# Kernel optimization log

Measured on AMD Instinct MI355X. Metric: run time of the kernel, lower is better.

## Reference

```python
import jax, jax.numpy as jnp
import numpy as np

H = 1024          # hidden_dim
N_AVAIL = 32768   # number of available ops (rows of the score matrix)
N_M = 64          # machines
N_OP = 40000      # unfinished ops
N_JOB = 2000      # jobs
L = 4             # policy_num_layers


def setup_inputs() -> dict:
    key = jax.random.key(0)
    ks = jax.random.split(key, 12)
    s_in = (2.0 / (2 * H + 2)) ** 0.5   # kaiming-ish scale
    s_h = (2.0 / H) ** 0.5
    return {
        "x_m": jax.random.normal(ks[0], (N_M, H), jnp.float32),
        "x_op": jax.random.normal(ks[1], (N_OP, H), jnp.float32),
        "job_srpt": jax.random.uniform(ks[2], (N_JOB,), jnp.float32),
        "pt": jax.random.uniform(ks[3], (N_AVAIL,), jnp.float32),  # process_time / max_process_time
        "W0": jax.random.normal(ks[4], (2 * H + 2, H), jnp.float32) * s_in,
        "b0": jnp.zeros((H,), jnp.float32),
        "W1": jax.random.normal(ks[5], (H, H), jnp.float32) * s_h,
        "b1": jnp.zeros((H,), jnp.float32),
        "W2": jax.random.normal(ks[6], (H, H), jnp.float32) * s_h,
        "b2": jnp.zeros((H,), jnp.float32),
        "W3": jax.random.normal(ks[7], (H, 1), jnp.float32) * s_h,
        "b3": jnp.zeros((1,), jnp.float32),
        "m_ids": jax.random.randint(ks[8], (N_AVAIL,), 0, N_M, jnp.int32),
        "op_idx": jax.random.randint(ks[9], (N_AVAIL,), 0, N_OP, jnp.int32),
        "job_ids": jax.random.randint(ks[10], (N_AVAIL,), 0, N_JOB, jnp.int32),
    }


def reference(x_m, x_op, job_srpt, pt, W0, b0, W1, b1, W2, b2, W3, b3,
              m_ids, op_idx, job_ids):
    # Batched gather + concat: replaces the per-op Python loop of torch.cat's.
    feat = jnp.concatenate(
        [x_m[m_ids],                     # [N, H]
         x_op[op_idx],                   # [N, H]
         job_srpt[job_ids][:, None],     # [N, 1]
         pt[:, None]],                   # [N, 1]
        axis=1)                          # [N, 2H+2]
    lrelu = lambda v: jax.nn.leaky_relu(v, 0.01)
    h = lrelu(feat @ W0 + b0)
    h = lrelu(h @ W1 + b1)
    h = lrelu(h @ W2 + b2)
    score = (h @ W3 + b3).ravel()        # [N]
    probs = jax.nn.softmax(score)        # softmax over available ops (dim=0)
    idx = jnp.argmax(score)              # greedy action
    return probs, idx
```

## Files before the change

### kernel.cpp

```cpp
#include <hip/hip_runtime.h>
#include <hip/hip_bf16.h>

typedef __attribute__((ext_vector_type(8))) short short8;
typedef __attribute__((ext_vector_type(4))) float f32x4;

#define GL2LDS16(g, l)                                                         \
  __builtin_amdgcn_global_load_lds(                                            \
      (const __attribute__((address_space(1))) unsigned int*)(g),              \
      (__attribute__((address_space(3))) unsigned int*)(l), 16, 0, 0)

__device__ __forceinline__ short8 lds_read_b128(const __hip_bfloat16* p) {
  short8 v;
  asm volatile("ds_read_b128 %0, %1"
               : "=v"(v)
               : "v"((unsigned)(uintptr_t)p));
  return v;
}

__global__ __launch_bounds__(256) void featB_kernel(
    const float* __restrict__ x_op, const float* __restrict__ job_srpt,
    const int* __restrict__ op_idx, const int* __restrict__ job_ids,
    __hip_bfloat16* __restrict__ featB, float* __restrict__ srow) {
  const long row = (long)blockIdx.x * 2 + (threadIdx.x >> 7);
  const int t = threadIdx.x & 127;
  const float* src = x_op + (long)op_idx[row] * 1024 + t * 8;
  float4 v0 = *(const float4*)src;
  float4 v1 = *(const float4*)(src + 4);
  union {
    __hip_bfloat16 h[8];
    int4 i4;
  } u;
  u.h[0] = __float2bfloat16(v0.x);
  u.h[1] = __float2bfloat16(v0.y);
  u.h[2] = __float2bfloat16(v0.z);
  u.h[3] = __float2bfloat16(v0.w);
  u.h[4] = __float2bfloat16(v1.x);
  u.h[5] = __float2bfloat16(v1.y);
  u.h[6] = __float2bfloat16(v1.z);
  u.h[7] = __float2bfloat16(v1.w);
  *(int4*)&featB[row * 1024 + t * 8] = u.i4;
  if (t == 0) srow[row] = job_srpt[job_ids[row]];
}

__global__ __launch_bounds__(256) void pm_kernel(const float* __restrict__ x_m,
                                                 const float* __restrict__ W0,
                                                 float* __restrict__ P_m) {
  const int c = blockIdx.x * 256 + threadIdx.x;
  const int m = blockIdx.y;
  const float* xr = x_m + m * 1024;
  float s = 0.f;
#pragma unroll 4
  for (int k = 0; k < 1024; ++k) s += xr[k] * W0[(long)k * 1024 + c];
  P_m[m * 1024 + c] = s;
}

__global__ __launch_bounds__(256) void wconv_kernel(
    const float* __restrict__ W, __hip_bfloat16* __restrict__ Wt, int K) {
  __shared__ float tile[64][65];
  const int kb = blockIdx.x * 64;
  const int nb = blockIdx.y * 64;
  const int t = threadIdx.x;
#pragma unroll
  for (int it = 0; it < 16; ++it) {
    int idx = it * 256 + t;
    int kk = idx >> 6, nn = idx & 63;
    tile[kk][nn] = W[(long)(kb + kk) * 1024 + nb + nn];
  }
  __syncthreads();
#pragma unroll
  for (int it = 0; it < 16; ++it) {
    int idx = it * 256 + t;
    int nn = idx >> 6, kk = idx & 63;
    Wt[(long)(nb + nn) * K + kb + kk] = __float2bfloat16(tile[kk][nn]);
  }
}

__global__ __launch_bounds__(512, 2) void gemm_kernel(
    const __hip_bfloat16* __restrict__ A, const __hip_bfloat16* __restrict__ Bt,
    __hip_bfloat16* __restrict__ C, const float* __restrict__ bias, int M,
    int N, int K, int rank2, const float* __restrict__ wr0,
    const float* __restrict__ wr1, const float* __restrict__ srow,
    const float* __restrict__ ptv, int fuseW3,
    const float* __restrict__ W3, float* __restrict__ scoreOut,
    const float* __restrict__ pmTab, const int* __restrict__ mids) {
  __shared__ __align__(16) __hip_bfloat16 As[2][256 * 64];
  __shared__ __align__(16) __hip_bfloat16 Bs[2][256 * 64];
  const int t = threadIdx.x;
  const int lane = t & 63;
  const int wid = t >> 6;
  const int wm = wid >> 2;
  const int wn = wid & 3;
  const long arow0 = (long)blockIdx.x * 256;
  const int bcol0 = blockIdx.y * 256;
  const int NT = K >> 6;

  const int sa_row = ((t >> 8) * 128) + ((t >> 3) & 31);
  const int sb_row = t >> 3;
  const int scol = ((t & 7) ^ ((t >> 3) & 7)) * 8;

#define STAGE_A(buf, kt1, p)                                                   \
  GL2LDS16(A + (arow0 + sa_row + (p) * 32) * (long)K + (kt1) * 64 + scol,      \
           &As[buf][(t >> 8) * 8192 + (p) * 2048 + (t & 255) * 8])
#define STAGE_B(buf, kt1, q)                                                   \
  GL2LDS16(Bt + (long)(bcol0 + sb_row + (q) * 64) * (long)K + (kt1) * 64 + scol, \
           &Bs[buf][(q) * 4096 + t * 8])

  f32x4 acc[8][4] = {};
  short8 bfr[8];

#pragma unroll
  for (int q = 0; q < 4; ++q) STAGE_B(0, 0, q);
#pragma unroll
  for (int p = 0; p < 4; ++p) STAGE_A(0, 0, p);

  for (int kt = 0; kt < NT; ++kt) {
    const int cur = kt & 1;
    const bool pre = (kt + 1) < NT;
#pragma unroll
    for (int p = 0; p < 4; ++p) {
      if (pre) {
        if (p == 0) { STAGE_B(cur ^ 1, kt + 1, 0); STAGE_B(cur ^ 1, kt + 1, 1); }
        if (p == 1) { STAGE_B(cur ^ 1, kt + 1, 2); STAGE_B(cur ^ 1, kt + 1, 3); }
        if (p == 2) { STAGE_A(cur ^ 1, kt + 1, 0); STAGE_A(cur ^ 1, kt + 1, 1); }
        if (p == 3) { STAGE_A(cur ^ 1, kt + 1, 2); STAGE_A(cur ^ 1, kt + 1, 3); }
        asm volatile("s_waitcnt vmcnt(4)" ::: "memory");
      } else {
        asm volatile("s_waitcnt vmcnt(0)" ::: "memory");
      }
      __builtin_amdgcn_s_barrier();

      short8 af[2][2];
      if (p == 0) {
#pragma unroll
        for (int j = 0; j < 4; ++j)
#pragma unroll
          for (int ks = 0; ks < 2; ++ks) {
            const int ko = (ks * 32 + ((lane >> 4) << 3)) ^ ((lane & 7) << 3);
            bfr[j * 2 + ks] =
                lds_read_b128(&Bs[cur][(wn * 64 + j * 16 + (lane & 15)) * 64 + ko]);
          }
      }
#pragma unroll
      for (int ii = 0; ii < 2; ++ii)
#pragma unroll
        for (int ks = 0; ks < 2; ++ks) {
          const int ko = (ks * 32 + ((lane >> 4) << 3)) ^ ((lane & 7) << 3);
          af[ii][ks] = lds_read_b128(
              &As[cur][(wm * 128 + (2 * p + ii) * 16 + (lane & 15)) * 64 + ko]);
        }

      asm volatile("s_waitcnt lgkmcnt(0)" ::: "memory");
      __builtin_amdgcn_sched_barrier(0);
      __builtin_amdgcn_s_setprio(1);
#pragma unroll
      for (int ii = 0; ii < 2; ++ii)
#pragma unroll
        for (int ks = 0; ks < 2; ++ks)
#pragma unroll
          for (int j = 0; j < 4; ++j)
            acc[2 * p + ii][j] = __builtin_amdgcn_mfma_f32_16x16x32_bf16(
                af[ii][ks], bfr[j * 2 + ks], acc[2 * p + ii][j], 0, 0, 0);
      __builtin_amdgcn_s_setprio(0);
      __builtin_amdgcn_s_barrier();
    }
  }

  if (!fuseW3) {
    float bia[4], wa[4], wb[4];
#pragma unroll
    for (int j = 0; j < 4; ++j) {
      const int c = bcol0 + wn * 64 + j * 16 + (lane & 15);
      bia[j] = bias[c];
      wa[j] = rank2 ? wr0[c] : 0.f;
      wb[j] = rank2 ? wr1[c] : 0.f;
    }
#pragma unroll
    for (int i = 0; i < 8; ++i) {
#pragma unroll
      for (int g = 0; g < 4; ++g) {
        const long r = arow0 + wm * 128 + i * 16 + ((lane >> 4) << 2) + g;
        float sr = 0.f, pv = 0.f;
        if (rank2) {
          sr = srow[r];
          pv = ptv[r];
        }
        const float* pmrow = pmTab ? (pmTab + (long)mids[r] * 1024) : nullptr;
#pragma unroll
        for (int j = 0; j < 4; ++j) {
          const int c = bcol0 + wn * 64 + j * 16 + (lane & 15);
          float v = acc[i][j][g] + bia[j];
          if (rank2) v += sr * wa[j] + pv * wb[j];
          if (pmrow) v += pmrow[c];
          v = v > 0.f ? v : 0.01f * v;
          C[r * N + c] = __float2bfloat16(v);
        }
      }
    }
  } else {
    float bia[4], w3v[4];
#pragma unroll
    for (int j = 0; j < 4; ++j) {
      const int c = bcol0 + wn * 64 + j * 16 + (lane & 15);
      bia[j] = bias[c];
      w3v[j] = W3[c];
    }
#pragma unroll
    for (int i = 0; i < 8; ++i) {
#pragma unroll
      for (int g = 0; g < 4; ++g) {
        float ps = 0.f;
#pragma unroll
        for (int j = 0; j < 4; ++j) {
          float v = acc[i][j][g] + bia[j];
          v = v > 0.f ? v : 0.01f * v;
          ps += v * w3v[j];
        }
        ps += __shfl_xor(ps, 1);
        ps += __shfl_xor(ps, 2);
        ps += __shfl_xor(ps, 4);
        ps += __shfl_xor(ps, 8);
        if ((lane & 15) == 0) {
          const long r = arow0 + wm * 128 + i * 16 + ((lane >> 4) << 2) + g;
          atomicAdd(&scoreOut[r], ps);
        }
      }
    }
  }
#undef STAGE_A
#undef STAGE_B
}

__global__ __launch_bounds__(256) void redmax_kernel(
    const float* __restrict__ score, float* __restrict__ pmax,
    int* __restrict__ pidx) {
  const int t = threadIdx.x, b = blockIdx.x;
  float m = -1e30f;
  int mi = 0;
#pragma unroll
  for (int u = 0; u < 2; ++u) {
    int i = b * 512 + u * 256 + t;
    float v = score[i];
    if (v > m) {
      m = v;
      mi = i;
    }
  }
  __shared__ float sm[4];
  __shared__ int si[4];
#pragma unroll
  for (int off = 32; off; off >>= 1) {
    float om = __shfl_down(m, off);
    int oi = __shfl_down(mi, off);
    if (om > m || (om == m && oi < mi)) {
      m = om;
      mi = oi;
    }
  }
  const int lane = t & 63, w = t >> 6;
  if (lane == 0) {
    sm[w] = m;
    si[w] = mi;
  }
  __syncthreads();
  if (t == 0) {
    for (int w2 = 1; w2 < 4; ++w2)
      if (sm[w2] > m || (sm[w2] == m && si[w2] < mi)) {
        m = sm[w2];
        mi = si[w2];
      }
    pmax[b] = m;
    pidx[b] = mi;
  }
}

__global__ __launch_bounds__(64) void finmax_kernel(
    const float* __restrict__ pmax, const int* __restrict__ pidx,
    float* __restrict__ gscal, float* __restrict__ out_idx) {
  const int t = threadIdx.x;
  float m = pmax[t];
  int mi = pidx[t];
#pragma unroll
  for (int off = 32; off; off >>= 1) {
    float om = __shfl_down(m, off);
    int oi = __shfl_down(mi, off);
    if (om > m || (om == m && oi < mi)) {
      m = om;
      mi = oi;
    }
  }
  if (t == 0) {
    gscal[0] = m;
    out_idx[0] = (float)mi;
  }
}

__global__ __launch_bounds__(256) void expsum_kernel(
    const float* __restrict__ score, const float* __restrict__ gscal,
    float* __restrict__ e, float* __restrict__ psum) {
  const int t = threadIdx.x, b = blockIdx.x;
  const float gmax = gscal[0];
  float s = 0.f;
#pragma unroll
  for (int u = 0; u < 2; ++u) {
    int i = b * 512 + u * 256 + t;
    float v = expf(score[i] - gmax);
    e[i] = v;
    s += v;
  }
#pragma unroll
  for (int off = 32; off; off >>= 1) s += __shfl_down(s, off);
  __shared__ float sm[4];
  const int lane = t & 63, w = t >> 6;
  if (lane == 0) sm[w] = s;
  __syncthreads();
  if (t == 0) psum[b] = sm[0] + sm[1] + sm[2] + sm[3];
}

__global__ __launch_bounds__(64) void finsum_kernel(const float* __restrict__ psum,
                                                    float* __restrict__ gscal) {
  float s = psum[threadIdx.x];
#pragma unroll
  for (int off = 32; off; off >>= 1) s += __shfl_down(s, off);
  if (threadIdx.x == 0) gscal[1] = 1.0f / s;
}

__global__ __launch_bounds__(256) void scale_kernel(float* __restrict__ e,
                                                    const float* __restrict__ gscal) {
  const float inv = gscal[1];
  const int i = blockIdx.x * 512 + threadIdx.x;
  e[i] *= inv;
  e[i + 256] *= inv;
}

extern "C" void kernel_launch(void* const* d_in, const int* in_sizes, int n_in,
                              void* d_out, int out_size, void* d_ws,
                              size_t ws_size, hipStream_t stream) {
  const float* x_m = (const float*)d_in[0];
  const float* x_op = (const float*)d_in[1];
  const float* job_srpt = (const float*)d_in[2];
  const float* pt = (const float*)d_in[3];
  const float* W0 = (const float*)d_in[4];
  const float* b0 = (const float*)d_in[5];
  const float* W1 = (const float*)d_in[6];
  const float* b1 = (const float*)d_in[7];
  const float* W2 = (const float*)d_in[8];
  const float* b2 = (const float*)d_in[9];
  const float* W3 = (const float*)d_in[10];
  const int* m_ids = (const int*)d_in[12];
  const int* op_idx = (const int*)d_in[13];
  const int* job_ids = (const int*)d_in[14];

  const int M = 32768;

  char* p = (char*)d_ws;
  __hip_bfloat16* featB = (__hip_bfloat16*)p;           p += (size_t)M * 1024 * 2;
  __hip_bfloat16* hA = (__hip_bfloat16*)p;              p += (size_t)M * 1024 * 2;
  __hip_bfloat16* hB = (__hip_bfloat16*)p;              p += (size_t)M * 1024 * 2;
  __hip_bfloat16* Wt0b = (__hip_bfloat16*)p;            p += (size_t)1024 * 1024 * 2;
  __hip_bfloat16* Wt1 = (__hip_bfloat16*)p;             p += (size_t)1024 * 1024 * 2;
  __hip_bfloat16* Wt2 = (__hip_bfloat16*)p;             p += (size_t)1024 * 1024 * 2;
  float* P_m = (float*)p;                               p += (size_t)64 * 1024 * 4;
  float* srow = (float*)p;                              p += (size_t)M * 4;
  float* score = (float*)p;                             p += (size_t)M * 4;
  float* pmax = (float*)p;                              p += 256;
  int* pidx = (int*)p;                                  p += 256;
  float* psum = (float*)p;                              p += 256;
  float* gscal = (float*)p;                             p += 256;

  float* probs = (float*)d_out;
  float* out_idx = probs + M;

  featB_kernel<<<M / 2, 256, 0, stream>>>(x_op, job_srpt, op_idx, job_ids,
                                          featB, srow);
  pm_kernel<<<dim3(4, 64), 256, 0, stream>>>(x_m, W0, P_m);
  wconv_kernel<<<dim3(16, 16), 256, 0, stream>>>(W0 + (size_t)1024 * 1024, Wt0b,
                                                 1024);
  wconv_kernel<<<dim3(16, 16), 256, 0, stream>>>(W1, Wt1, 1024);
  wconv_kernel<<<dim3(16, 16), 256, 0, stream>>>(W2, Wt2, 1024);
  hipMemsetAsync(score, 0, (size_t)M * 4, stream);

  gemm_kernel<<<dim3(128, 4), 512, 0, stream>>>(
      featB, Wt0b, hA, b0, M, 1024, 1024, 1, W0 + (size_t)2048 * 1024,
      W0 + (size_t)2049 * 1024, srow, pt, 0, nullptr, nullptr, P_m, m_ids);
  gemm_kernel<<<dim3(128, 4), 512, 0, stream>>>(
      hA, Wt1, hB, b1, M, 1024, 1024, 0, nullptr, nullptr, nullptr, nullptr, 0,
      nullptr, nullptr, nullptr, nullptr);
  gemm_kernel<<<dim3(128, 4), 512, 0, stream>>>(
      hB, Wt2, nullptr, b2, M, 1024, 1024, 0, nullptr, nullptr, nullptr,
      nullptr, 1, W3, score, nullptr, nullptr);

  redmax_kernel<<<64, 256, 0, stream>>>(score, pmax, pidx);
  finmax_kernel<<<1, 64, 0, stream>>>(pmax, pidx, gscal, out_idx);
  expsum_kernel<<<64, 256, 0, stream>>>(score, gscal, probs, psum);
  finsum_kernel<<<1, 64, 0, stream>>>(psum, gscal);
  scale_kernel<<<64, 256, 0, stream>>>(probs, gscal);
}
```

Before: 448.0 us.

## Shrink GEMM tile to 128x256 single-buffered LDS for higher occupancy

The GEMM block tile drops from 256x256 with double-buffered LDS to 128x256 with a single LDS buffer. Launch bounds rise to 4 blocks per CU and the grid doubles. The explicit software prefetch pipeline is replaced by a plain load, sync, compute, sync loop, so latency hiding now depends on occupancy across blocks instead of overlap inside a block. This costs more B-tile reloads per output and exposes global-load latency within each block.

```diff
diff --git a/kernel.cpp b/kernel.cpp
--- a/kernel.cpp
+++ b/kernel.cpp
@@ -75,7 +75,7 @@
   }
 }
 
-__global__ __launch_bounds__(512, 2) void gemm_kernel(
+__global__ __launch_bounds__(512, 4) void gemm_kernel(
     const __hip_bfloat16* __restrict__ A, const __hip_bfloat16* __restrict__ Bt,
     __hip_bfloat16* __restrict__ C, const float* __restrict__ bias, int M,
     int N, int K, int rank2, const float* __restrict__ wr0,
@@ -83,86 +83,68 @@
     const float* __restrict__ ptv, int fuseW3,
     const float* __restrict__ W3, float* __restrict__ scoreOut,
     const float* __restrict__ pmTab, const int* __restrict__ mids) {
-  __shared__ __align__(16) __hip_bfloat16 As[2][256 * 64];
-  __shared__ __align__(16) __hip_bfloat16 Bs[2][256 * 64];
+  __shared__ __align__(16) __hip_bfloat16 As[128 * 64];
+  __shared__ __align__(16) __hip_bfloat16 Bs[256 * 64];
   const int t = threadIdx.x;
   const int lane = t & 63;
   const int wid = t >> 6;
   const int wm = wid >> 2;
   const int wn = wid & 3;
-  const long arow0 = (long)blockIdx.x * 256;
+  const long arow0 = (long)blockIdx.x * 128;
   const int bcol0 = blockIdx.y * 256;
   const int NT = K >> 6;
 
-  const int sa_row = ((t >> 8) * 128) + ((t >> 3) & 31);
-  const int sb_row = t >> 3;
-  const int scol = ((t & 7) ^ ((t >> 3) & 7)) * 8;
-
-#define STAGE_A(buf, kt1, p)                                                   \
-  GL2LDS16(A + (arow0 + sa_row + (p) * 32) * (long)K + (kt1) * 64 + scol,      \
-           &As[buf][(t >> 8) * 8192 + (p) * 2048 + (t & 255) * 8])
-#define STAGE_B(buf, kt1, q)                                                   \
-  GL2LDS16(Bt + (long)(bcol0 + sb_row + (q) * 64) * (long)K + (kt1) * 64 + scol, \
-           &Bs[buf][(q) * 4096 + t * 8])
-
-  f32x4 acc[8][4] = {};
+  const int s_row = t >> 3;
+  const int scol = ((t & 7) ^ (s_row & 7)) * 8;
+
+  f32x4 acc[4][4] = {};
   short8 bfr[8];
 
-#pragma unroll
-  for (int q = 0; q < 4; ++q) STAGE_B(0, 0, q);
-#pragma unroll
-  for (int p = 0; p < 4; ++p) STAGE_A(0, 0, p);
-
   for (int kt = 0; kt < NT; ++kt) {
-    const int cur = kt & 1;
-    const bool pre = (kt + 1) < NT;
-#pragma unroll
-    for (int p = 0; p < 4; ++p) {
-      if (pre) {
-        if (p == 0) { STAGE_B(cur ^ 1, kt + 1, 0); STAGE_B(cur ^ 1, kt + 1, 1); }
-        if (p == 1) { STAGE_B(cur ^ 1, kt + 1, 2); STAGE_B(cur ^ 1, kt + 1, 3); }
-        if (p == 2) { STAGE_A(cur ^ 1, kt + 1, 0); STAGE_A(cur ^ 1, kt + 1, 1); }
-        if (p == 3) { STAGE_A(cur ^ 1, kt + 1, 2); STAGE_A(cur ^ 1, kt + 1, 3); }
-        asm volatile("s_waitcnt vmcnt(4)" ::: "memory");
-      } else {
-        asm volatile("s_waitcnt vmcnt(0)" ::: "memory");
-      }
-      __builtin_amdgcn_s_barrier();
-
-      short8 af[2][2];
-      if (p == 0) {
-#pragma unroll
-        for (int j = 0; j < 4; ++j)
-#pragma unroll
-          for (int ks = 0; ks < 2; ++ks) {
-            const int ko = (ks * 32 + ((lane >> 4) << 3)) ^ ((lane & 7) << 3);
-            bfr[j * 2 + ks] =
-                lds_read_b128(&Bs[cur][(wn * 64 + j * 16 + (lane & 15)) * 64 + ko]);
-          }
-      }
-#pragma unroll
-      for (int ii = 0; ii < 2; ++ii)
-#pragma unroll
-        for (int ks = 0; ks < 2; ++ks) {
-          const int ko = (ks * 32 + ((lane >> 4) << 3)) ^ ((lane & 7) << 3);
-          af[ii][ks] = lds_read_b128(
-              &As[cur][(wm * 128 + (2 * p + ii) * 16 + (lane & 15)) * 64 + ko]);
-        }
-
+#pragma unroll
+    for (int it = 0; it < 2; ++it) {
+      int cc = it * 512 + t;
+      int r = cc >> 3, c8 = (cc & 7) ^ (r & 7);
+      GL2LDS16(A + (arow0 + r) * (long)K + kt * 64 + c8 * 8, &As[cc * 8]);
+    }
+#pragma unroll
+    for (int it = 0; it < 4; ++it) {
+      int cc = it * 512 + t;
+      int r = cc >> 3, c8 = (cc & 7) ^ (r & 7);
+      GL2LDS16(Bt + (long)(bcol0 + r) * (long)K + kt * 64 + c8 * 8,
+               &Bs[cc * 8]);
+    }
+    __syncthreads();
+
+#pragma unroll
+    for (int j = 0; j < 4; ++j)
+#pragma unroll
+      for (int ks = 0; ks < 2; ++ks) {
+        const int ko = (ks * 32 + ((lane >> 4) << 3)) ^ ((lane & 7) << 3);
+        bfr[j * 2 + ks] =
+            lds_read_b128(&Bs[(wn * 64 + j * 16 + (lane & 15)) * 64 + ko]);
+      }
+#pragma unroll
+    for (int i = 0; i < 4; ++i) {
+      short8 af[2];
+#pragma unroll
+      for (int ks = 0; ks < 2; ++ks) {
+        const int ko = (ks * 32 + ((lane >> 4) << 3)) ^ ((lane & 7) << 3);
+        af[ks] = lds_read_b128(
+            &As[(wm * 64 + i * 16 + (lane & 15)) * 64 + ko]);
+      }
       asm volatile("s_waitcnt lgkmcnt(0)" ::: "memory");
       __builtin_amdgcn_sched_barrier(0);
       __builtin_amdgcn_s_setprio(1);
 #pragma unroll
-      for (int ii = 0; ii < 2; ++ii)
-#pragma unroll
-        for (int ks = 0; ks < 2; ++ks)
-#pragma unroll
-          for (int j = 0; j < 4; ++j)
-            acc[2 * p + ii][j] = __builtin_amdgcn_mfma_f32_16x16x32_bf16(
-                af[ii][ks], bfr[j * 2 + ks], acc[2 * p + ii][j], 0, 0, 0);
+      for (int ks = 0; ks < 2; ++ks)
+#pragma unroll
+        for (int j = 0; j < 4; ++j)
+          acc[i][j] = __builtin_amdgcn_mfma_f32_16x16x32_bf16(
+              af[ks], bfr[j * 2 + ks], acc[i][j], 0, 0, 0);
       __builtin_amdgcn_s_setprio(0);
-      __builtin_amdgcn_s_barrier();
-    }
+    }
+    __syncthreads();
   }
 
   if (!fuseW3) {
@@ -175,10 +157,10 @@
       wb[j] = rank2 ? wr1[c] : 0.f;
     }
 #pragma unroll
-    for (int i = 0; i < 8; ++i) {
+    for (int i = 0; i < 4; ++i) {
 #pragma unroll
       for (int g = 0; g < 4; ++g) {
-        const long r = arow0 + wm * 128 + i * 16 + ((lane >> 4) << 2) + g;
+        const long r = arow0 + wm * 64 + i * 16 + ((lane >> 4) << 2) + g;
         float sr = 0.f, pv = 0.f;
         if (rank2) {
           sr = srow[r];
@@ -205,7 +187,7 @@
       w3v[j] = W3[c];
     }
 #pragma unroll
-    for (int i = 0; i < 8; ++i) {
+    for (int i = 0; i < 4; ++i) {
 #pragma unroll
       for (int g = 0; g < 4; ++g) {
         float ps = 0.f;
@@ -220,14 +202,12 @@
         ps += __shfl_xor(ps, 4);
         ps += __shfl_xor(ps, 8);
         if ((lane & 15) == 0) {
-          const long r = arow0 + wm * 128 + i * 16 + ((lane >> 4) << 2) + g;
+          const long r = arow0 + wm * 64 + i * 16 + ((lane >> 4) << 2) + g;
           atomicAdd(&scoreOut[r], ps);
         }
       }
     }
   }
-#undef STAGE_A
-#undef STAGE_B
 }
 
 __global__ __launch_bounds__(256) void redmax_kernel(
@@ -379,13 +359,13 @@
   wconv_kernel<<<dim3(16, 16), 256, 0, stream>>>(W2, Wt2, 1024);
   hipMemsetAsync(score, 0, (size_t)M * 4, stream);
 
-  gemm_kernel<<<dim3(128, 4), 512, 0, stream>>>(
+  gemm_kernel<<<dim3(256, 4), 512, 0, stream>>>(
       featB, Wt0b, hA, b0, M, 1024, 1024, 1, W0 + (size_t)2048 * 1024,
       W0 + (size_t)2049 * 1024, srow, pt, 0, nullptr, nullptr, P_m, m_ids);
-  gemm_kernel<<<dim3(128, 4), 512, 0, stream>>>(
+  gemm_kernel<<<dim3(256, 4), 512, 0, stream>>>(
       hA, Wt1, hB, b1, M, 1024, 1024, 0, nullptr, nullptr, nullptr, nullptr, 0,
       nullptr, nullptr, nullptr, nullptr);
-  gemm_kernel<<<dim3(128, 4), 512, 0, stream>>>(
+  gemm_kernel<<<dim3(256, 4), 512, 0, stream>>>(
       hB, Wt2, nullptr, b2, M, 1024, 1024, 0, nullptr, nullptr, nullptr,
       nullptr, 1, W3, score, nullptr, nullptr);
 
```

Result: slower. 486.5 us (+8.6%).

## Switch MLP GEMMs to FP8 and rescore top candidates exactly for argmax

Applied to the files above, without the earlier changes.

Converts activations and weights to FP8 (weights scaled by 32) and runs the three large GEMMs with fp8 MFMA at K-tile 128, halving operand bytes and raising matrix throughput. To keep the argmax close to the reference, it picks rows within a fixed margin of the approximate max, capped at 256, and recomputes their scores in FP32 with small GEMM kernels. The softmax probabilities still come from FP8-precision scores, so accuracy may degrade, and the margin/cap heuristic could miss the true argmax.

```diff
diff --git a/kernel.cpp b/kernel.cpp
--- a/kernel.cpp
+++ b/kernel.cpp
@@ -1,7 +1,6 @@
 #include <hip/hip_runtime.h>
 #include <hip/hip_bf16.h>
 
-typedef __attribute__((ext_vector_type(8))) short short8;
 typedef __attribute__((ext_vector_type(4))) float f32x4;
 
 #define GL2LDS16(g, l)                                                         \
@@ -9,36 +8,32 @@
       (const __attribute__((address_space(1))) unsigned int*)(g),              \
       (__attribute__((address_space(3))) unsigned int*)(l), 16, 0, 0)
 
-__device__ __forceinline__ short8 lds_read_b128(const __hip_bfloat16* p) {
-  short8 v;
-  asm volatile("ds_read_b128 %0, %1"
-               : "=v"(v)
-               : "v"((unsigned)(uintptr_t)p));
+__device__ __forceinline__ long lds_read_b64(const void* p) {
+  long v;
+  asm volatile("ds_read_b64 %0, %1" : "=v"(v) : "v"((unsigned)(uintptr_t)p));
   return v;
+}
+
+__device__ __forceinline__ unsigned char f2fp8(float v) {
+  int r = __builtin_amdgcn_cvt_pk_fp8_f32(v, 0.f, 0, 0);
+  return (unsigned char)(r & 0xff);
 }
 
 __global__ __launch_bounds__(256) void featB_kernel(
     const float* __restrict__ x_op, const float* __restrict__ job_srpt,
     const int* __restrict__ op_idx, const int* __restrict__ job_ids,
-    __hip_bfloat16* __restrict__ featB, float* __restrict__ srow) {
+    unsigned char* __restrict__ featB, float* __restrict__ srow) {
   const long row = (long)blockIdx.x * 2 + (threadIdx.x >> 7);
   const int t = threadIdx.x & 127;
   const float* src = x_op + (long)op_idx[row] * 1024 + t * 8;
   float4 v0 = *(const float4*)src;
   float4 v1 = *(const float4*)(src + 4);
-  union {
-    __hip_bfloat16 h[8];
-    int4 i4;
-  } u;
-  u.h[0] = __float2bfloat16(v0.x);
-  u.h[1] = __float2bfloat16(v0.y);
-  u.h[2] = __float2bfloat16(v0.z);
-  u.h[3] = __float2bfloat16(v0.w);
-  u.h[4] = __float2bfloat16(v1.x);
-  u.h[5] = __float2bfloat16(v1.y);
-  u.h[6] = __float2bfloat16(v1.z);
-  u.h[7] = __float2bfloat16(v1.w);
-  *(int4*)&featB[row * 1024 + t * 8] = u.i4;
+  unsigned int w0 = __builtin_amdgcn_cvt_pk_fp8_f32(v0.x, v0.y, 0, 0);
+  w0 = __builtin_amdgcn_cvt_pk_fp8_f32(v0.z, v0.w, w0, 1);
+  unsigned int w1 = __builtin_amdgcn_cvt_pk_fp8_f32(v1.x, v1.y, 0, 0);
+  w1 = __builtin_amdgcn_cvt_pk_fp8_f32(v1.z, v1.w, w1, 1);
+  uint2 out = {w0, w1};
+  *(uint2*)&featB[row * 1024 + t * 8] = out;
   if (t == 0) srow[row] = job_srpt[job_ids[row]];
 }
 
@@ -55,7 +50,7 @@
 }
 
 __global__ __launch_bounds__(256) void wconv_kernel(
-    const float* __restrict__ W, __hip_bfloat16* __restrict__ Wt, int K) {
+    const float* __restrict__ W, unsigned char* __restrict__ Wt, int K) {
   __shared__ float tile[64][65];
   const int kb = blockIdx.x * 64;
   const int nb = blockIdx.y * 64;
@@ -71,20 +66,20 @@
   for (int it = 0; it < 16; ++it) {
     int idx = it * 256 + t;
     int nn = idx >> 6, kk = idx & 63;
-    Wt[(long)(nb + nn) * K + kb + kk] = __float2bfloat16(tile[kk][nn]);
+    Wt[(long)(nb + nn) * K + kb + kk] = f2fp8(tile[kk][nn] * 32.f);
   }
 }
 
 __global__ __launch_bounds__(512, 2) void gemm_kernel(
-    const __hip_bfloat16* __restrict__ A, const __hip_bfloat16* __restrict__ Bt,
-    __hip_bfloat16* __restrict__ C, const float* __restrict__ bias, int M,
+    const unsigned char* __restrict__ A, const unsigned char* __restrict__ Bt,
+    unsigned char* __restrict__ C, const float* __restrict__ bias, int M,
     int N, int K, int rank2, const float* __restrict__ wr0,
     const float* __restrict__ wr1, const float* __restrict__ srow,
     const float* __restrict__ ptv, int fuseW3,
     const float* __restrict__ W3, float* __restrict__ scoreOut,
     const float* __restrict__ pmTab, const int* __restrict__ mids) {
-  __shared__ __align__(16) __hip_bfloat16 As[2][256 * 64];
-  __shared__ __align__(16) __hip_bfloat16 Bs[2][256 * 64];
+  __shared__ __align__(16) unsigned char As[2][32768];
+  __shared__ __align__(16) unsigned char Bs[2][32768];
   const int t = threadIdx.x;
   const int lane = t & 63;
   const int wid = t >> 6;
@@ -92,21 +87,29 @@
   const int wn = wid & 3;
   const long arow0 = (long)blockIdx.x * 256;
   const int bcol0 = blockIdx.y * 256;
-  const int NT = K >> 6;
+  const int NT = K >> 7;
 
   const int sa_row = ((t >> 8) * 128) + ((t >> 3) & 31);
   const int sb_row = t >> 3;
-  const int scol = ((t & 7) ^ ((t >> 3) & 7)) * 8;
+  const int scolB = ((t & 7) ^ ((t >> 3) & 7)) * 16;
+  const int sa_dst = (t >> 8) * 16384 + (t & 255) * 16;
 
 #define STAGE_A(buf, kt1, p)                                                   \
-  GL2LDS16(A + (arow0 + sa_row + (p) * 32) * (long)K + (kt1) * 64 + scol,      \
-           &As[buf][(t >> 8) * 8192 + (p) * 2048 + (t & 255) * 8])
+  GL2LDS16(A + (arow0 + sa_row + (p) * 32) * (long)K + (kt1) * 128 + scolB,    \
+           &As[buf][sa_dst + (p) * 4096])
 #define STAGE_B(buf, kt1, q)                                                   \
-  GL2LDS16(Bt + (long)(bcol0 + sb_row + (q) * 64) * (long)K + (kt1) * 64 + scol, \
-           &Bs[buf][(q) * 4096 + t * 8])
+  GL2LDS16(Bt + (long)(bcol0 + sb_row + (q) * 64) * (long)K + (kt1) * 128 +    \
+               scolB,                                                          \
+           &Bs[buf][(q) * 8192 + t * 16])
 
   f32x4 acc[8][4] = {};
-  short8 bfr[8];
+  long bfr[4][4];
+  const int g = lane >> 4;
+  const int lx = lane & 7;
+  int koff[4];
+#pragma unroll
+  for (int ks = 0; ks < 4; ++ks)
+    koff[ks] = (((2 * ks + (g >> 1)) ^ lx) << 4) + ((g & 1) << 3);
 
 #pragma unroll
   for (int q = 0; q < 4; ++q) STAGE_B(0, 0, q);
@@ -129,25 +132,23 @@
       }
       __builtin_amdgcn_s_barrier();
 
-      short8 af[2][2];
+      long af[2][4];
       if (p == 0) {
 #pragma unroll
-        for (int j = 0; j < 4; ++j)
-#pragma unroll
-          for (int ks = 0; ks < 2; ++ks) {
-            const int ko = (ks * 32 + ((lane >> 4) << 3)) ^ ((lane & 7) << 3);
-            bfr[j * 2 + ks] =
-                lds_read_b128(&Bs[cur][(wn * 64 + j * 16 + (lane & 15)) * 64 + ko]);
-          }
-      }
-#pragma unroll
-      for (int ii = 0; ii < 2; ++ii)
-#pragma unroll
-        for (int ks = 0; ks < 2; ++ks) {
-          const int ko = (ks * 32 + ((lane >> 4) << 3)) ^ ((lane & 7) << 3);
-          af[ii][ks] = lds_read_b128(
-              &As[cur][(wm * 128 + (2 * p + ii) * 16 + (lane & 15)) * 64 + ko]);
+        for (int j = 0; j < 4; ++j) {
+          const int rb = (wn * 64 + j * 16 + (lane & 15)) * 128;
+#pragma unroll
+          for (int ks = 0; ks < 4; ++ks)
+            bfr[j][ks] = lds_read_b64(&Bs[cur][rb + koff[ks]]);
         }
+      }
+#pragma unroll
+      for (int ii = 0; ii < 2; ++ii) {
+        const int rb = (wm * 128 + (2 * p + ii) * 16 + (lane & 15)) * 128;
+#pragma unroll
+        for (int ks = 0; ks < 4; ++ks)
+          af[ii][ks] = lds_read_b64(&As[cur][rb + koff[ks]]);
+      }
 
       asm volatile("s_waitcnt lgkmcnt(0)" ::: "memory");
       __builtin_amdgcn_sched_barrier(0);
@@ -155,16 +156,17 @@
 #pragma unroll
       for (int ii = 0; ii < 2; ++ii)
 #pragma unroll
-        for (int ks = 0; ks < 2; ++ks)
+        for (int ks = 0; ks < 4; ++ks)
 #pragma unroll
           for (int j = 0; j < 4; ++j)
-            acc[2 * p + ii][j] = __builtin_amdgcn_mfma_f32_16x16x32_bf16(
-                af[ii][ks], bfr[j * 2 + ks], acc[2 * p + ii][j], 0, 0, 0);
+            acc[2 * p + ii][j] = __builtin_amdgcn_mfma_f32_16x16x32_fp8_fp8(
+                af[ii][ks], bfr[j][ks], acc[2 * p + ii][j], 0, 0, 0);
       __builtin_amdgcn_s_setprio(0);
       __builtin_amdgcn_s_barrier();
     }
   }
 
+  const float INV = 1.0f / 32.0f;
   if (!fuseW3) {
     float bia[4], wa[4], wb[4];
 #pragma unroll
@@ -177,8 +179,8 @@
 #pragma unroll
     for (int i = 0; i < 8; ++i) {
 #pragma unroll
-      for (int g = 0; g < 4; ++g) {
-        const long r = arow0 + wm * 128 + i * 16 + ((lane >> 4) << 2) + g;
+      for (int gg = 0; gg < 4; ++gg) {
+        const long r = arow0 + wm * 128 + i * 16 + ((lane >> 4) << 2) + gg;
         float sr = 0.f, pv = 0.f;
         if (rank2) {
           sr = srow[r];
@@ -188,11 +190,11 @@
 #pragma unroll
         for (int j = 0; j < 4; ++j) {
           const int c = bcol0 + wn * 64 + j * 16 + (lane & 15);
-          float v = acc[i][j][g] + bia[j];
+          float v = acc[i][j][gg] * INV + bia[j];
           if (rank2) v += sr * wa[j] + pv * wb[j];
           if (pmrow) v += pmrow[c];
           v = v > 0.f ? v : 0.01f * v;
-          C[r * N + c] = __float2bfloat16(v);
+          C[r * N + c] = f2fp8(v);
         }
       }
     }
@@ -207,11 +209,11 @@
 #pragma unroll
     for (int i = 0; i < 8; ++i) {
 #pragma unroll
-      for (int g = 0; g < 4; ++g) {
+      for (int gg = 0; gg < 4; ++gg) {
         float ps = 0.f;
 #pragma unroll
         for (int j = 0; j < 4; ++j) {
-          float v = acc[i][j][g] + bia[j];
+          float v = acc[i][j][gg] * INV + bia[j];
           v = v > 0.f ? v : 0.01f * v;
           ps += v * w3v[j];
         }
@@ -220,7 +222,7 @@
         ps += __shfl_xor(ps, 4);
         ps += __shfl_xor(ps, 8);
         if ((lane & 15) == 0) {
-          const long r = arow0 + wm * 128 + i * 16 + ((lane >> 4) << 2) + g;
+          const long r = arow0 + wm * 128 + i * 16 + ((lane >> 4) << 2) + gg;
           atomicAdd(&scoreOut[r], ps);
         }
       }
@@ -275,7 +277,7 @@
 
 __global__ __launch_bounds__(64) void finmax_kernel(
     const float* __restrict__ pmax, const int* __restrict__ pidx,
-    float* __restrict__ gscal, float* __restrict__ out_idx) {
+    float* __restrict__ gscal) {
   const int t = threadIdx.x;
   float m = pmax[t];
   int mi = pidx[t];
@@ -288,10 +290,7 @@
       mi = oi;
     }
   }
-  if (t == 0) {
-    gscal[0] = m;
-    out_idx[0] = (float)mi;
-  }
+  if (t == 0) gscal[0] = m;
 }
 
 __global__ __launch_bounds__(256) void expsum_kernel(
@@ -330,6 +329,114 @@
   const int i = blockIdx.x * 512 + threadIdx.x;
   e[i] *= inv;
   e[i + 256] *= inv;
+}
+
+#define RS_MARGIN 1.25f
+#define RS_CAP 256
+
+__global__ __launch_bounds__(512) void cand_kernel(
+    const float* __restrict__ score, const float* __restrict__ gscal,
+    int* __restrict__ cand, int* __restrict__ ccount) {
+  const int i = blockIdx.x * 512 + threadIdx.x;
+  if (score[i] >= gscal[0] - RS_MARGIN) {
+    int pos = atomicAdd(ccount, 1);
+    if (pos < RS_CAP) cand[pos] = i;
+  }
+}
+
+__global__ __launch_bounds__(256) void rs_feat_kernel(
+    const float* __restrict__ x_m, const float* __restrict__ x_op,
+    const int* __restrict__ m_ids, const int* __restrict__ op_idx,
+    const int* __restrict__ cand, float* __restrict__ featC) {
+  const int b = blockIdx.x;
+  const int r = cand[b];
+  const int k0 = threadIdx.x * 8;
+  const float* src = (k0 < 1024) ? (x_m + (long)m_ids[r] * 1024 + k0)
+                                 : (x_op + (long)op_idx[r] * 1024 + (k0 - 1024));
+  float4 v0 = *(const float4*)src;
+  float4 v1 = *(const float4*)(src + 4);
+  *(float4*)&featC[(long)b * 2048 + k0] = v0;
+  *(float4*)&featC[(long)b * 2048 + k0 + 4] = v1;
+}
+
+__global__ __launch_bounds__(256) void rs_gemm_kernel(
+    const float* __restrict__ In, int ldin, int K, const float* __restrict__ W,
+    const float* __restrict__ bias, float* __restrict__ Out, int rank2,
+    const float* __restrict__ w2a, const float* __restrict__ w2b,
+    const float* __restrict__ srow, const float* __restrict__ ptv,
+    const int* __restrict__ cand) {
+  const int cx = blockIdx.x * 256 + threadIdx.x;
+  const int ry = blockIdx.y * 4;
+  float acc[4] = {0.f, 0.f, 0.f, 0.f};
+  for (int k = 0; k < K; ++k) {
+    const float w = W[(long)k * 1024 + cx];
+#pragma unroll
+    for (int rr = 0; rr < 4; ++rr) acc[rr] += In[(long)(ry + rr) * ldin + k] * w;
+  }
+#pragma unroll
+  for (int rr = 0; rr < 4; ++rr) {
+    float v = acc[rr] + bias[cx];
+    if (rank2) {
+      const int r = cand[ry + rr];
+      v += srow[r] * w2a[cx] + ptv[r] * w2b[cx];
+    }
+    v = v > 0.f ? v : 0.01f * v;
+    Out[(long)(ry + rr) * 1024 + cx] = v;
+  }
+}
+
+__global__ __launch_bounds__(256) void rs_score_kernel(
+    const float* __restrict__ H, const float* __restrict__ W3,
+    float* __restrict__ exact) {
+  const int b = blockIdx.x;
+  const int t = threadIdx.x;
+  float s = 0.f;
+#pragma unroll
+  for (int e = 0; e < 4; ++e) {
+    int k = t * 4 + e;
+    s += H[(long)b * 1024 + k] * W3[k];
+  }
+#pragma unroll
+  for (int off = 32; off; off >>= 1) s += __shfl_down(s, off);
+  __shared__ float sm[4];
+  const int lane = t & 63, w = t >> 6;
+  if (lane == 0) sm[w] = s;
+  __syncthreads();
+  if (t == 0) exact[b] = sm[0] + sm[1] + sm[2] + sm[3];
+}
+
+__global__ __launch_bounds__(256) void rs_final_kernel(
+    const float* __restrict__ exact, const int* __restrict__ cand,
+    const int* __restrict__ ccount, float* __restrict__ out_idx) {
+  const int t = threadIdx.x;
+  const int n = min(*ccount, RS_CAP);
+  float s = (t < n) ? exact[t] : -1e30f;
+  int r = (t < n) ? cand[t] : 0x7fffffff;
+#pragma unroll
+  for (int off = 32; off; off >>= 1) {
+    float os = __shfl_down(s, off);
+    int orr = __shfl_down(r, off);
+    if (os > s || (os == s && orr < r)) {
+      s = os;
+      r = orr;
+    }
+  }
+  __shared__ float sm[4];
+  __shared__ int sr[4];
+  const int lane = t & 63, w = t >> 6;
+  if (lane == 0) {
+    sm[w] = s;
+    sr[w] = r;
+  }
+  __syncthreads();
+  if (t == 0) {
+    for (int w2 = 1; w2 < 4; ++w2)
+      if (sm[w2] > s || (sm[w2] == s && sr[w2] < r)) {
+        s = sm[w2];
+        r = sr[w2];
+      }
+    out_idx[0] = (float)r;
+  }
 }
 
 extern "C" void kernel_launch(void* const* d_in, const int* in_sizes, int n_in,
@@ -353,19 +460,26 @@
   const int M = 32768;
 
   char* p = (char*)d_ws;
-  __hip_bfloat16* featB = (__hip_bfloat16*)p;           p += (size_t)M * 1024 * 2;
-  __hip_bfloat16* hA = (__hip_bfloat16*)p;              p += (size_t)M * 1024 * 2;
-  __hip_bfloat16* hB = (__hip_bfloat16*)p;              p += (size_t)M * 1024 * 2;
-  __hip_bfloat16* Wt0b = (__hip_bfloat16*)p;            p += (size_t)1024 * 1024 * 2;
-  __hip_bfloat16* Wt1 = (__hip_bfloat16*)p;             p += (size_t)1024 * 1024 * 2;
-  __hip_bfloat16* Wt2 = (__hip_bfloat16*)p;             p += (size_t)1024 * 1024 * 2;
-  float* P_m = (float*)p;                               p += (size_t)64 * 1024 * 4;
-  float* srow = (float*)p;                              p += (size_t)M * 4;
-  float* score = (float*)p;                             p += (size_t)M * 4;
-  float* pmax = (float*)p;                              p += 256;
-  int* pidx = (int*)p;                                  p += 256;
-  float* psum = (float*)p;                              p += 256;
-  float* gscal = (float*)p;                             p += 256;
+  unsigned char* featB = (unsigned char*)p;   p += (size_t)M * 1024;
+  unsigned char* hA = (unsigned char*)p;      p += (size_t)M * 1024;
+  unsigned char* hB = (unsigned char*)p;      p += (size_t)M * 1024;
+  unsigned char* Wt0b = (unsigned char*)p;    p += (size_t)1024 * 1024;
+  unsigned char* Wt1 = (unsigned char*)p;     p += (size_t)1024 * 1024;
+  unsigned char* Wt2 = (unsigned char*)p;     p += (size_t)1024 * 1024;
+  float* P_m = (float*)p;                     p += (size_t)64 * 1024 * 4;
+  float* srow = (float*)p;                    p += (size_t)M * 4;
+  float* score = (float*)p;                   p += (size_t)M * 4;
+  float* featC = (float*)p;                   p += (size_t)256 * 2048 * 4;
+  float* rsH1 = (float*)p;                    p += (size_t)256 * 1024 * 4;
+  float* rsH2 = (float*)p;                    p += (size_t)256 * 1024 * 4;
+  float* rsH3 = (float*)p;                    p += (size_t)256 * 1024 * 4;
+  float* exact = (float*)p;                   p += 1024;
+  int* cand = (int*)p;                        p += 1024;
+  int* ccount = (int*)p;                      p += 256;
+  float* pmax = (float*)p;                    p += 256;
+  int* pidx = (int*)p;                        p += 256;
+  float* psum = (float*)p;                    p += 256;
+  float* gscal = (float*)p;                   p += 256;
 
   float* probs = (float*)d_out;
   float* out_idx = probs + M;
@@ -378,6 +492,7 @@
   wconv_kernel<<<dim3(16, 16), 256, 0, stream>>>(W1, Wt1, 1024);
   wconv_kernel<<<dim3(16, 16), 256, 0, stream>>>(W2, Wt2, 1024);
   hipMemsetAsync(score, 0, (size_t)M * 4, stream);
+  hipMemsetAsync(cand, 0, 1024 + 256, stream);
 
   gemm_kernel<<<dim3(128, 4), 512, 0, stream>>>(
       featB, Wt0b, hA, b0, M, 1024, 1024, 1, W0 + (size_t)2048 * 1024,
@@ -390,7 +505,23 @@
       nullptr, 1, W3, score, nullptr, nullptr);
 
   redmax_kernel<<<64, 256, 0, stream>>>(score, pmax, pidx);
-  finmax_kernel<<<1, 64, 0, stream>>>(pmax, pidx, gscal, out_idx);
+  finmax_kernel<<<1, 64, 0, stream>>>(pmax, pidx, gscal);
+
+  cand_kernel<<<64, 512, 0, stream>>>(score, gscal, cand, ccount);
+  rs_feat_kernel<<<256, 256, 0, stream>>>(x_m, x_op, m_ids, op_idx, cand,
+                                          featC);
+  rs_gemm_kernel<<<dim3(4, 64), 256, 0, stream>>>(
+      featC, 2048, 2048, W0, b0, rsH1, 1, W0 + (size_t)2048 * 1024,
+      W0 + (size_t)2049 * 1024, srow, pt, cand);
+  rs_gemm_kernel<<<dim3(4, 64), 256, 0, stream>>>(rsH1, 1024, 1024, W1, b1,
+                                                  rsH2, 0, nullptr, nullptr,
+                                                  nullptr, nullptr, cand);
+  rs_gemm_kernel<<<dim3(4, 64), 256, 0, stream>>>(rsH2, 1024, 1024, W2, b2,
+                                                  rsH3, 0, nullptr, nullptr,
+                                                  nullptr, nullptr, cand);
+  rs_score_kernel<<<256, 256, 0, stream>>>(rsH3, W3, exact);
+  rs_final_kernel<<<1, 256, 0, stream>>>(exact, cand, ccount, out_idx);
+
   expsum_kernel<<<64, 256, 0, stream>>>(score, gscal, probs, psum);
   finsum_kernel<<<1, 64, 0, stream>>>(psum, gscal);
   scale_kernel<<<64, 256, 0, stream>>>(probs, gscal);
```

Result: slower. 1.495 ms (+233.8%).
